# Performance work log

Measured on AMD Instinct MI355X. Metric: run time of the kernel, lower is better.

The kernel has to match this reference:

```python
import jax, jax.numpy as jnp
import numpy as np

N_CLASSES = 3  # hardcoded in the original module (labels == 0/1/2)
EPS = 1e-12    # F.normalize default eps


def setup_inputs() -> dict:
    key = jax.random.key(0)
    k1, k2, k3 = jax.random.split(key, 3)
    query = jax.random.normal(k1, (32768, 256), dtype=jnp.float32)
    memory = jax.random.normal(k2, (3, 512, 256), dtype=jnp.float32)
    labels = jax.random.randint(k3, (32768,), 0, 3, dtype=jnp.int64)
    return {"query": query, "labels": labels, "memory": memory}


def reference(query, labels, memory):
    C, n_cells, d = memory.shape  # (3, 512, 256)
    # ---- read: cross-attention over all C*n_cells memory slots ----
    mem_flat = memory.reshape(C * n_cells, d)
    scores = jax.nn.softmax(query @ mem_flat.T, axis=1)  # (N, C*n_cells)
    q_read = scores @ mem_flat                           # (N, d) == the per-row loop, batched

    # ---- update (training path): masked softmax over queries per class ----
    def upd(c):
        mask = labels == c                               # (N,)
        logits = query @ memory[c].T                     # (N, n_cells)
        logits = jnp.where(mask[:, None], logits, -jnp.inf)
        sq = jax.nn.softmax(logits, axis=0)              # softmax over (masked) queries
        delta = sq.T @ query                             # (n_cells, d); zero rows contribute 0
        new = memory[c] + delta
        norm = jnp.maximum(jnp.linalg.norm(new, axis=1, keepdims=True), EPS)
        return new / norm                                # F.normalize over dim=1

    new_mem = jnp.stack([upd(c) for c in range(C)])      # C is a small fixed constant (3)
    return q_read, jax.lax.stop_gradient(new_mem)        # original detaches updated memory
```

## Files before the change

### kernel.cpp

```cpp
#include <hip/hip_runtime.h>
#include <math.h>

#define NQ    32768
#define DDIM  256
#define NCLS  3
#define CELLS 512
#define STOT  1536
#define BK    32

typedef __attribute__((ext_vector_type(8)))  short bf16x8;
typedef __attribute__((ext_vector_type(16))) float f32x16;

#define ROWF(r) (((r) & 3) + 8 * ((r) >> 2) + 4 * lh)

#define PIPE_WAIT_BAR(N) asm volatile("s_waitcnt vmcnt(" #N ")\n\ts_barrier" ::: "memory")
#define PIPE_BAR()       asm volatile("s_barrier" ::: "memory")

__device__ __forceinline__ f32x16 mfma16(bf16x8 a, bf16x8 b, f32x16 c) {
    return __builtin_amdgcn_mfma_f32_32x32x16_bf16(a, b, c, 0, 0, 0);
}
__device__ __forceinline__ unsigned short f2bf(float f) {
    const unsigned u = __float_as_uint(f);
    return (unsigned short)((u + 0x7FFFu + ((u >> 16) & 1u)) >> 16);
}
__device__ __forceinline__ float bf2f(unsigned short b) {
    return __uint_as_float(((unsigned)b) << 16);
}
__device__ __forceinline__ float sum16(bf16x8 w0, bf16x8 w1) {
    float s = 0.f;
#pragma unroll
    for (int e = 0; e < 8; ++e)
        s += bf2f((unsigned short)w0[e]) + bf2f((unsigned short)w1[e]);
    return s;
}
__device__ __forceinline__ void gl16(const unsigned short* g, unsigned short* l) {
    __builtin_amdgcn_global_load_lds(
        (const __attribute__((address_space(1))) unsigned int*)g,
        (__attribute__((address_space(3))) unsigned int*)l, 16, 0, 0);
}

__global__ __launch_bounds__(256) void k_conv2(const float* __restrict__ Q,
        const float* __restrict__ M,
        unsigned short* __restrict__ Qhi, unsigned short* __restrict__ Qlo,
        unsigned short* __restrict__ QhiT, float* __restrict__ qn2,
        unsigned short* __restrict__ Mhi, unsigned short* __restrict__ Mlo,
        unsigned short* __restrict__ MhiT, float* __restrict__ mn2) {
    __shared__ unsigned short lh_s[64][65];
    const int bq = NQ / 64;
    const bool isQ = (int)blockIdx.x < bq;
    const float* src        = isQ ? Q    : M;
    unsigned short* hi      = isQ ? Qhi  : Mhi;
    unsigned short* lo      = isQ ? Qlo  : Mlo;
    unsigned short* hiT     = isQ ? QhiT : MhiT;
    float* sq               = isQ ? qn2  : mn2;
    const int R             = isQ ? NQ   : STOT;
    const int r0 = (isQ ? blockIdx.x : blockIdx.x - bq) * 64;
    const int k0 = blockIdx.y * 64, t = threadIdx.x;
#pragma unroll
    for (int it = 0; it < 4; ++it) {
        const int idx = t + 256 * it;
        const int rl = idx >> 4, kq = idx & 15;
        const float4 v = *(const float4*)(src + (size_t)(r0 + rl) * DDIM + k0 + kq * 4);
        const unsigned short h0 = f2bf(v.x), h1 = f2bf(v.y), h2 = f2bf(v.z), h3 = f2bf(v.w);
        const unsigned short l0 = f2bf(v.x - bf2f(h0)), l1 = f2bf(v.y - bf2f(h1));
        const unsigned short l2 = f2bf(v.z - bf2f(h2)), l3 = f2bf(v.w - bf2f(h3));
        ushort4 hv; hv.x = h0; hv.y = h1; hv.z = h2; hv.w = h3;
        ushort4 lv; lv.x = l0; lv.y = l1; lv.z = l2; lv.w = l3;
        *(ushort4*)(hi + (size_t)(r0 + rl) * DDIM + k0 + kq * 4) = hv;
        *(ushort4*)(lo + (size_t)(r0 + rl) * DDIM + k0 + kq * 4) = lv;
        lh_s[rl][kq * 4 + 0] = h0; lh_s[rl][kq * 4 + 1] = h1;
        lh_s[rl][kq * 4 + 2] = h2; lh_s[rl][kq * 4 + 3] = h3;
        float ssq = v.x * v.x + v.y * v.y + v.z * v.z + v.w * v.w;
        ssq += __shfl_xor(ssq, 1, 64);
        ssq += __shfl_xor(ssq, 2, 64);
        ssq += __shfl_xor(ssq, 4, 64);
        ssq += __shfl_xor(ssq, 8, 64);
        if (kq == 0) atomicAdd(&sq[r0 + rl], ssq);
    }
    __syncthreads();
#pragma unroll
    for (int it = 0; it < 16; ++it) {
        const int idx = t + 256 * it;
        const int kl = idx >> 6, rl = idx & 63;
        hiT[(size_t)(k0 + kl) * R + r0 + rl] = lh_s[rl][kl];
    }
}

__global__ __launch_bounds__(256) void k_pe(
        const unsigned short* __restrict__ Qhi, const unsigned short* __restrict__ Qlo,
        const unsigned short* __restrict__ Mhi, const unsigned short* __restrict__ Mlo,
        const int* __restrict__ labels, const float* __restrict__ qn2,
        const float* __restrict__ mn2,
        unsigned short* __restrict__ P, unsigned short* __restrict__ ET,
        float* __restrict__ rowsum, float* __restrict__ colsum,
        int ibase, int ch, int ipg) {
    __shared__ unsigned short sA[2][2][128][BK];
    __shared__ unsigned short sB[2][2][192][BK];
    typedef unsigned short trt[32][40];
    trt* trP = (trt*)&sA[0][0][0][0];
    trt* trE = trP + 4;

    const int t = threadIdx.x, lane = t & 63, wid = t >> 6;
    const int l31 = lane & 31, lh = lane >> 5;
    const int wi = wid >> 1, wj = wid & 1;
    int ib, jb;
    if (ipg > 0) {
        const int xcd = blockIdx.x & 7, s = blockIdx.x >> 3;
        jb = s & 7; ib = xcd * ipg + (s >> 3);
    } else { jb = blockIdx.x % 8; ib = blockIdx.x / 8; }
    const int iblk = ib * 128, jblk = jb * 192;
    const int iloc0 = iblk + wi * 64;
    const int j0    = jblk + wj * 96;

    const unsigned short* gA[2] = { Qhi + (size_t)(ibase + iblk) * DDIM,
                                    Qlo + (size_t)(ibase + iblk) * DDIM };
    const unsigned short* gB[2] = { Mhi + (size_t)jblk * DDIM,
                                    Mlo + (size_t)jblk * DDIM };
    auto STAGE = [&](int b, int k0) {
#pragma unroll
        for (int h = 0; h < 2; ++h) {
#pragma unroll
            for (int it = 0; it < 2; ++it) {
                const int c = wid * 128 + it * 64 + lane;
                const int r = c >> 2, o = ((c ^ (c >> 3)) & 3) * 8;
                gl16(gA[h] + (size_t)r * DDIM + k0 + o, &sA[b][h][0][0] + c * 8);
            }
#pragma unroll
            for (int it = 0; it < 3; ++it) {
                const int c = wid * 192 + it * 64 + lane;
                const int r = c >> 2, o = ((c ^ (c >> 3)) & 3) * 8;
                gl16(gB[h] + (size_t)r * DDIM + k0 + o, &sB[b][h][0][0] + c * 8);
            }
        }
    };

    f32x16 acc[2][3] = {};
    const int ra0 = wi * 64 + l31, ra1 = ra0 + 32;
    const int rb0 = wj * 96 + l31, rb1 = rb0 + 32, rb2 = rb0 + 64;
    const int swa = (ra0 >> 1) & 3;
    const int swb = (rb0 >> 1) & 3;
    auto COMPUTE = [&](int b) {
#pragma unroll
        for (int t16 = 0; t16 < 2; ++t16) {
            const int oc = t16 * 2 + lh;
            const int ka = (oc ^ swa) * 8, kb = (oc ^ swb) * 8;
            const bf16x8 a0h = *(const bf16x8*)&sA[b][0][ra0][ka];
            const bf16x8 a1h = *(const bf16x8*)&sA[b][0][ra1][ka];
            const bf16x8 a0l = *(const bf16x8*)&sA[b][1][ra0][ka];
            const bf16x8 a1l = *(const bf16x8*)&sA[b][1][ra1][ka];
            const bf16x8 b0h = *(const bf16x8*)&sB[b][0][rb0][kb];
            const bf16x8 b1h = *(const bf16x8*)&sB[b][0][rb1][kb];
            const bf16x8 b2h = *(const bf16x8*)&sB[b][0][rb2][kb];
            const bf16x8 b0l = *(const bf16x8*)&sB[b][1][rb0][kb];
            const bf16x8 b1l = *(const bf16x8*)&sB[b][1][rb1][kb];
            const bf16x8 b2l = *(const bf16x8*)&sB[b][1][rb2][kb];
            acc[0][0] = mfma16(a0h, b0h, acc[0][0]);
            acc[0][0] = mfma16(a0h, b0l, acc[0][0]);
            acc[0][0] = mfma16(a0l, b0h, acc[0][0]);
            acc[0][1] = mfma16(a0h, b1h, acc[0][1]);
            acc[0][1] = mfma16(a0h, b1l, acc[0][1]);
            acc[0][1] = mfma16(a0l, b1h, acc[0][1]);
            acc[0][2] = mfma16(a0h, b2h, acc[0][2]);
            acc[0][2] = mfma16(a0h, b2l, acc[0][2]);
            acc[0][2] = mfma16(a0l, b2h, acc[0][2]);
            acc[1][0] = mfma16(a1h, b0h, acc[1][0]);
            acc[1][0] = mfma16(a1h, b0l, acc[1][0]);
            acc[1][0] = mfma16(a1l, b0h, acc[1][0]);
            acc[1][1] = mfma16(a1h, b1h, acc[1][1]);
            acc[1][1] = mfma16(a1h, b1l, acc[1][1]);
            acc[1][1] = mfma16(a1l, b1h, acc[1][1]);
            acc[1][2] = mfma16(a1h, b2h, acc[1][2]);
            acc[1][2] = mfma16(a1h, b2l, acc[1][2]);
            acc[1][2] = mfma16(a1l, b2h, acc[1][2]);
        }
    };

    STAGE(0, 0);
    STAGE(1, BK);
    for (int s = 0; s < DDIM / BK - 1; ++s) {
        PIPE_WAIT_BAR(10);
        COMPUTE(s & 1);
        PIPE_BAR();
        if (s + 2 < DDIM / BK) STAGE(s & 1, (s + 2) * BK);
    }
    PIPE_WAIT_BAR(0);
    COMPUTE(1);
    __syncthreads();

    float em3[3];
#pragma unroll
    for (int tj = 0; tj < 3; ++tj)
        em3[tj] = __expf(96.0f - 6.0f * sqrtf(mn2[j0 + tj * 32 + l31]));

    float rsum[2] = {0.f, 0.f};
    float csum[3] = {0.f, 0.f, 0.f};
#pragma unroll
    for (int ti = 0; ti < 2; ++ti) {
        float qn[16], eq[16]; int lab[16];
        const int ig0 = ibase + iloc0 + ti * 32;
#pragma unroll
        for (int r = 0; r < 16; ++r) {
            const int ir = ig0 + ROWF(r);
            qn[r] = 6.0f * sqrtf(qn2[ir]);
            eq[r] = __expf(qn[r] - 96.0f);
            lab[r] = labels[ir];
        }
#pragma unroll
        for (int tj = 0; tj < 3; ++tj) {
            const int cblk = (j0 + tj * 32) >> 9;
            const float em = em3[tj];
#pragma unroll
            for (int r = 0; r < 16; r += 2) {
                const float p0 = __expf(acc[ti][tj][r] - qn[r]);
                const float p1 = __expf(acc[ti][tj][r + 1] - qn[r + 1]);
                trP[wid][ROWF(r)][l31]     = f2bf(p0);
                trP[wid][ROWF(r + 1)][l31] = f2bf(p1);
                const float e0 = (lab[r] == cblk)     ? p0 * eq[r] * em     : 0.0f;
                const float e1 = (lab[r + 1] == cblk) ? p1 * eq[r + 1] * em : 0.0f;
                const unsigned pk = (unsigned)f2bf(e0) | ((unsigned)f2bf(e1) << 16);
                *(unsigned*)&trE[wid][l31][ROWF(r)] = pk;
            }
            const int rr = lane >> 1, off = (lane & 1) * 16;
            {
                const unsigned short* lp = &trP[wid][rr][off];
                const bf16x8 w0 = *(const bf16x8*)(lp);
                const bf16x8 w1 = *(const bf16x8*)(lp + 8);
                unsigned short* prow = P + (size_t)(iloc0 + ti * 32 + rr) * STOT
                                         + j0 + tj * 32 + off;
                *(bf16x8*)(prow)     = w0;
                *(bf16x8*)(prow + 8) = w1;
                rsum[ti] += sum16(w0, w1);
            }
            {
                const unsigned short* lp = &trE[wid][rr][off];
                const bf16x8 w0 = *(const bf16x8*)(lp);
                const bf16x8 w1 = *(const bf16x8*)(lp + 8);
                unsigned short* erow = ET + (size_t)(j0 + tj * 32 + rr) * ch
                                          + iloc0 + ti * 32 + off;
                *(bf16x8*)(erow)     = w0;
                *(bf16x8*)(erow + 8) = w1;
                csum[tj] += sum16(w0, w1);
            }
        }
    }
    {
        const int rr = lane >> 1;
#pragma unroll
        for (int ti = 0; ti < 2; ++ti) {
            const float v = rsum[ti] + __shfl_xor(rsum[ti], 1, 64);
            if ((lane & 1) == 0)
                atomicAdd(&rowsum[ibase + iloc0 + ti * 32 + rr], v);
        }
#pragma unroll
        for (int tj = 0; tj < 3; ++tj) {
            const float v = csum[tj] + __shfl_xor(csum[tj], 1, 64);
            if ((lane & 1) == 0)
                atomicAdd(&colsum[j0 + tj * 32 + rr], v);
        }
    }
}

__global__ __launch_bounds__(256) void k_pv(const unsigned short* __restrict__ P,
        const unsigned short* __restrict__ MhiT, const float* __restrict__ rowsum,
        float* __restrict__ out, int ibase) {
    __shared__ unsigned short sP[2][128][64];
    __shared__ unsigned short sV[2][128][64];
    const int t = threadIdx.x, lane = t & 63, wid = t >> 6;
    const int l31 = lane & 31, lh = lane >> 5;
    const int wq = wid >> 1, wd = wid & 1;
    const int qblk = blockIdx.x * 128, dblk = blockIdx.y * 128;
    const unsigned short* gP = P + (size_t)qblk * STOT;
    const unsigned short* gV = MhiT + (size_t)dblk * STOT;

    auto STAGE = [&](int b, int k0) {
#pragma unroll
        for (int it = 0; it < 4; ++it) {
            const int c = wid * 256 + it * 64 + lane;
            const int r = c >> 3, o = ((c & 7) ^ (r & 7)) * 8;
            gl16(gP + (size_t)r * STOT + k0 + o, &sP[b][0][0] + c * 8);
            gl16(gV + (size_t)r * STOT + k0 + o, &sV[b][0][0] + c * 8);
        }
    };

    f32x16 acc[2][2] = {};
    const int rp0 = wq * 64 + l31, rp1 = rp0 + 32;
    const int rv0 = wd * 64 + l31, rv1 = rv0 + 32;
    auto COMPUTE = [&](int b) {
#pragma unroll
        for (int t16 = 0; t16 < 4; ++t16) {
            const int oc = t16 * 2 + lh;
            const bf16x8 a0 = *(const bf16x8*)&sP[b][rp0][(oc ^ (rp0 & 7)) * 8];
            const bf16x8 a1 = *(const bf16x8*)&sP[b][rp1][(oc ^ (rp1 & 7)) * 8];
            const bf16x8 b0 = *(const bf16x8*)&sV[b][rv0][(oc ^ (rv0 & 7)) * 8];
            const bf16x8 b1 = *(const bf16x8*)&sV[b][rv1][(oc ^ (rv1 & 7)) * 8];
            acc[0][0] = mfma16(a0, b0, acc[0][0]);
            acc[0][1] = mfma16(a0, b1, acc[0][1]);
            acc[1][0] = mfma16(a1, b0, acc[1][0]);
            acc[1][1] = mfma16(a1, b1, acc[1][1]);
        }
    };

    STAGE(0, 0);
    STAGE(1, 64);
    for (int s = 0; s < STOT / 64 - 1; ++s) {
        PIPE_WAIT_BAR(8);
        COMPUTE(s & 1);
        PIPE_BAR();
        if (s + 2 < STOT / 64) STAGE(s & 1, (s + 2) * 64);
    }
    PIPE_WAIT_BAR(0);
    COMPUTE(1);

    float riv[2][16];
#pragma unroll
    for (int tq = 0; tq < 2; ++tq)
#pragma unroll
        for (int r = 0; r < 16; ++r)
            riv[tq][r] = 1.f / rowsum[ibase + qblk + wq * 64 + tq * 32 + ROWF(r)];
#pragma unroll
    for (int tq = 0; tq < 2; ++tq) {
#pragma unroll
        for (int td = 0; td < 2; ++td) {
#pragma unroll
            for (int r = 0; r < 16; ++r) {
                const int ig = ibase + qblk + wq * 64 + tq * 32 + ROWF(r);
                const int od = dblk + wd * 64 + td * 32 + l31;
                out[(size_t)ig * DDIM + od] = acc[tq][td][r] * riv[tq][r];
            }
        }
    }
}

__global__ __launch_bounds__(256) void k_delta4(const unsigned short* __restrict__ ET,
        const unsigned short* __restrict__ QhiT,
        float* __restrict__ delta, int ibase, int ch, int ppx) {
    __shared__ unsigned short sE[2][128][64];
    __shared__ unsigned short sQ[2][128][64];
    const int t = threadIdx.x, lane = t & 63, wid = t >> 6;
    const int l31 = lane & 31, lh = lane >> 5;
    const int wj = wid >> 1, wd = wid & 1;
    int jb, db, kb;
    if (ppx > 0) {
        const int xcd = blockIdx.x & 7, s = blockIdx.x >> 3;
        jb = s % 12;
        const int pidx = xcd * ppx + s / 12;
        kb = pidx >> 1; db = pidx & 1;
    } else {
        jb = blockIdx.x % 12; db = (blockIdx.x / 12) & 1; kb = blockIdx.x / 24;
    }
    const int jblk = jb * 128, dblk = db * 128, i0 = kb * 1024;
    const int j0 = jblk + wj * 64, d0 = dblk + wd * 64;
    const unsigned short* gE = ET + (size_t)jblk * ch + i0;
    const unsigned short* gQ = QhiT + (size_t)dblk * NQ + ibase + i0;

    auto STAGE = [&](int b, int k0) {
#pragma unroll
        for (int it = 0; it < 4; ++it) {
            const int c = wid * 256 + it * 64 + lane;
            const int r = c >> 3, o = ((c & 7) ^ (r & 7)) * 8;
            gl16(gE + (size_t)r * ch + k0 + o, &sE[b][0][0] + c * 8);
            gl16(gQ + (size_t)r * NQ + k0 + o, &sQ[b][0][0] + c * 8);
        }
    };

    f32x16 acc[2][2] = {};
    const int re0 = wj * 64 + l31, re1 = re0 + 32;
    const int rq0 = wd * 64 + l31, rq1 = rq0 + 32;
    auto COMPUTE = [&](int b) {
#pragma unroll
        for (int t16 = 0; t16 < 4; ++t16) {
            const int oc = t16 * 2 + lh;
            const bf16x8 a0 = *(const bf16x8*)&sE[b][re0][(oc ^ (re0 & 7)) * 8];
            const bf16x8 a1 = *(const bf16x8*)&sE[b][re1][(oc ^ (re1 & 7)) * 8];
            const bf16x8 b0 = *(const bf16x8*)&sQ[b][rq0][(oc ^ (rq0 & 7)) * 8];
            const bf16x8 b1 = *(const bf16x8*)&sQ[b][rq1][(oc ^ (rq1 & 7)) * 8];
            acc[0][0] = mfma16(a0, b0, acc[0][0]);
            acc[0][1] = mfma16(a0, b1, acc[0][1]);
            acc[1][0] = mfma16(a1, b0, acc[1][0]);
            acc[1][1] = mfma16(a1, b1, acc[1][1]);
        }
    };

    STAGE(0, 0);
    STAGE(1, 64);
    for (int s = 0; s < 15; ++s) {
        PIPE_WAIT_BAR(8);
        COMPUTE(s & 1);
        PIPE_BAR();
        if (s + 2 < 16) STAGE(s & 1, (s + 2) * 64);
    }
    PIPE_WAIT_BAR(0);
    COMPUTE(1);

#pragma unroll
    for (int tj = 0; tj < 2; ++tj) {
#pragma unroll
        for (int td = 0; td < 2; ++td) {
#pragma unroll
            for (int r = 0; r < 16; ++r) {
                const int jr = j0 + tj * 32 + ROWF(r);
                atomicAdd(&delta[(size_t)jr * DDIM + d0 + td * 32 + l31], acc[tj][td][r]);
            }
        }
    }
}

__global__ void k_final(const float* __restrict__ M,
                        const float* __restrict__ delta,
                        const float* __restrict__ colsum,
                        float* __restrict__ out) {
    const int row  = blockIdx.x * 4 + (threadIdx.x >> 6);
    const int lane = threadIdx.x & 63;
    const float inv = 1.f / colsum[row];
    const float4 mv = *(const float4*)(M + (size_t)row * DDIM + lane * 4);
    const float4 dv = *(const float4*)(delta + (size_t)row * DDIM + lane * 4);
    float4 nv;
    nv.x = fmaf(dv.x, inv, mv.x);
    nv.y = fmaf(dv.y, inv, mv.y);
    nv.z = fmaf(dv.z, inv, mv.z);
    nv.w = fmaf(dv.w, inv, mv.w);
    float ss = nv.x * nv.x + nv.y * nv.y + nv.z * nv.z + nv.w * nv.w;
#pragma unroll
    for (int sh = 1; sh < 64; sh <<= 1) ss += __shfl_xor(ss, sh, 64);
    const float rn = 1.f / fmaxf(sqrtf(ss), 1e-12f);
    nv.x *= rn; nv.y *= rn; nv.z *= rn; nv.w *= rn;
    *(float4*)(out + (size_t)NQ * DDIM + (size_t)row * DDIM + lane * 4) = nv;
}

extern "C" void kernel_launch(void* const* d_in, const int* in_sizes, int n_in,
                              void* d_out, int out_size, void* d_ws, size_t ws_size,
                              hipStream_t stream) {
    const float* Q      = (const float*)d_in[0];
    const int*   labels = (const int*)d_in[1];
    const float* M      = (const float*)d_in[2];
    float* out = (float*)d_out;

    char* p = (char*)d_ws;
    float* colsum = (float*)p;          p += (size_t)STOT * 4;
    float* delta  = (float*)p;          p += (size_t)STOT * DDIM * 4;
    float* qn2    = (float*)p;          p += (size_t)NQ * 4;
    float* mn2    = (float*)p;          p += (size_t)STOT * 4;
    float* rowsum = (float*)p;          p += (size_t)NQ * 4;
    const size_t zero_bytes = (size_t)(p - (char*)d_ws);
    unsigned short* Qhi  = (unsigned short*)p; p += (size_t)NQ * DDIM * 2;
    unsigned short* Qlo  = (unsigned short*)p; p += (size_t)NQ * DDIM * 2;
    unsigned short* QhiT = (unsigned short*)p; p += (size_t)NQ * DDIM * 2;
    unsigned short* Mhi  = (unsigned short*)p; p += (size_t)STOT * DDIM * 2;
    unsigned short* Mlo  = (unsigned short*)p; p += (size_t)STOT * DDIM * 2;
    unsigned short* MhiT = (unsigned short*)p; p += (size_t)STOT * DDIM * 2;
    const size_t fixed_bytes = (size_t)(p - (char*)d_ws);

    int nch = 2;
    while (nch < 32 &&
           fixed_bytes + (size_t)(NQ / nch) * STOT * 2 * 2 > ws_size) nch <<= 1;
    const int ch = NQ / nch;
    unsigned short* Pbuf = (unsigned short*)p;
    unsigned short* ETb  = Pbuf + (size_t)ch * STOT;

    const int ipg    = ((ch / 128) % 8 == 0) ? (ch / 128) / 8 : 0;
    const int ksplit = ch / 1024;
    const int ppx    = ((2 * ksplit) % 8 == 0) ? (2 * ksplit) / 8 : 0;

    hipMemsetAsync(d_ws, 0, zero_bytes, stream);

    k_conv2<<<dim3(NQ / 64 + STOT / 64, 4), 256, 0, stream>>>(
        Q, M, Qhi, Qlo, QhiT, qn2, Mhi, Mlo, MhiT, mn2);

    for (int h = 0; h < nch; ++h) {
        const int ibase = h * ch;
        k_pe<<<8 * (ch / 128), 256, 0, stream>>>(Qhi, Qlo, Mhi, Mlo, labels,
                                                 qn2, mn2, Pbuf, ETb, rowsum, colsum,
                                                 ibase, ch, ipg);
        k_pv<<<dim3(ch / 128, 2), 256, 0, stream>>>(Pbuf, MhiT, rowsum, out, ibase);
        k_delta4<<<24 * ksplit, 256, 0, stream>>>(ETb, QhiT, delta, ibase, ch, ppx);
    }
    k_final<<<STOT / 4, 256, 0, stream>>>(M, delta, colsum, out);
}
```

Measured before the change: 266.4 us.

## Sort queries by label so delta GEMM skips zero-masked class blocks

Adds count and scatter kernels that build a label-sorted permutation of queries. Conversion gathers query rows in that order, and the PV output is scattered back through the index. The E matrix and the delta GEMM then touch only the contiguous K-range of each class's queries, which cuts that GEMM's work to about a third. It costs two extra small launches and atomics, an indirect output write, and a delta split that may be uneven across K.

```diff
diff --git a/kernel.cpp b/kernel.cpp
--- a/kernel.cpp
+++ b/kernel.cpp
@@ -39,8 +39,46 @@
         (__attribute__((address_space(3))) unsigned int*)l, 16, 0, 0);
 }
 
+__global__ __launch_bounds__(256) void k_count(const int* __restrict__ labels,
+        unsigned* __restrict__ cnt) {
+    const int i = blockIdx.x * 256 + threadIdx.x;
+    const int lane = threadIdx.x & 63;
+    const int c = labels[i];
+    const unsigned long long m0 = __ballot(c == 0), m1 = __ballot(c == 1);
+    if (lane == 0) {
+        const unsigned n0 = __popcll(m0), n1 = __popcll(m1);
+        atomicAdd(&cnt[0], n0);
+        atomicAdd(&cnt[1], n1);
+        atomicAdd(&cnt[2], 64u - n0 - n1);
+    }
+}
+
+__global__ __launch_bounds__(256) void k_scatter(const int* __restrict__ labels,
+        const unsigned* __restrict__ cnt, unsigned* __restrict__ wcnt,
+        int* __restrict__ idx) {
+    const int i = blockIdx.x * 256 + threadIdx.x;
+    const int lane = threadIdx.x & 63;
+    const int c = labels[i];
+    const unsigned long long m0 = __ballot(c == 0), m1 = __ballot(c == 1),
+                             m2 = __ballot(c == 2);
+    const unsigned long long mym = (c == 0) ? m0 : (c == 1) ? m1 : m2;
+    const unsigned long long ltm = ((unsigned long long)1 << lane) - 1;
+    const unsigned rank = __popcll(mym & ltm);
+    int b0 = 0, b1 = 0, b2 = 0;
+    if (lane == 0) {
+        b0 = (int)atomicAdd(&wcnt[0], __popcll(m0));
+        b1 = (int)atomicAdd(&wcnt[1], __popcll(m1));
+        b2 = (int)atomicAdd(&wcnt[2], __popcll(m2));
+    }
+    b0 = __shfl(b0, 0, 64); b1 = __shfl(b1, 0, 64); b2 = __shfl(b2, 0, 64);
+    const unsigned base = (c == 0) ? (unsigned)b0
+                        : (c == 1) ? cnt[0] + (unsigned)b1
+                                   : cnt[0] + cnt[1] + (unsigned)b2;
+    idx[base + rank] = i;
+}
+
 __global__ __launch_bounds__(256) void k_conv2(const float* __restrict__ Q,
-        const float* __restrict__ M,
+        const float* __restrict__ M, const int* __restrict__ idx,
         unsigned short* __restrict__ Qhi, unsigned short* __restrict__ Qlo,
         unsigned short* __restrict__ QhiT, float* __restrict__ qn2,
         unsigned short* __restrict__ Mhi, unsigned short* __restrict__ Mlo,
@@ -58,9 +96,10 @@
     const int k0 = blockIdx.y * 64, t = threadIdx.x;
 #pragma unroll
     for (int it = 0; it < 4; ++it) {
-        const int idx = t + 256 * it;
-        const int rl = idx >> 4, kq = idx & 15;
-        const float4 v = *(const float4*)(src + (size_t)(r0 + rl) * DDIM + k0 + kq * 4);
+        const int idxl = t + 256 * it;
+        const int rl = idxl >> 4, kq = idxl & 15;
+        const int orow = isQ ? idx[r0 + rl] : (r0 + rl);
+        const float4 v = *(const float4*)(src + (size_t)orow * DDIM + k0 + kq * 4);
         const unsigned short h0 = f2bf(v.x), h1 = f2bf(v.y), h2 = f2bf(v.z), h3 = f2bf(v.w);
         const unsigned short l0 = f2bf(v.x - bf2f(h0)), l1 = f2bf(v.y - bf2f(h1));
         const unsigned short l2 = f2bf(v.z - bf2f(h2)), l3 = f2bf(v.w - bf2f(h3));
@@ -80,8 +119,8 @@
     __syncthreads();
 #pragma unroll
     for (int it = 0; it < 16; ++it) {
-        const int idx = t + 256 * it;
-        const int kl = idx >> 6, rl = idx & 63;
+        const int idxl = t + 256 * it;
+        const int kl = idxl >> 6, rl = idxl & 63;
         hiT[(size_t)(k0 + kl) * R + r0 + rl] = lh_s[rl][kl];
     }
 }
@@ -89,7 +128,7 @@
 __global__ __launch_bounds__(256) void k_pe(
         const unsigned short* __restrict__ Qhi, const unsigned short* __restrict__ Qlo,
         const unsigned short* __restrict__ Mhi, const unsigned short* __restrict__ Mlo,
-        const int* __restrict__ labels, const float* __restrict__ qn2,
+        const unsigned* __restrict__ cnt, const float* __restrict__ qn2,
         const float* __restrict__ mn2,
         unsigned short* __restrict__ P, unsigned short* __restrict__ ET,
         float* __restrict__ rowsum, float* __restrict__ colsum,
@@ -187,6 +226,7 @@
     COMPUTE(1);
     __syncthreads();
 
+    const int sC1 = (int)cnt[0], sC2 = sC1 + (int)cnt[1];
     float em3[3];
 #pragma unroll
     for (int tj = 0; tj < 3; ++tj)
@@ -196,18 +236,23 @@
     float csum[3] = {0.f, 0.f, 0.f};
 #pragma unroll
     for (int ti = 0; ti < 2; ++ti) {
-        float qn[16], eq[16]; int lab[16];
+        float qn[16], eq[16];
         const int ig0 = ibase + iloc0 + ti * 32;
 #pragma unroll
         for (int r = 0; r < 16; ++r) {
             const int ir = ig0 + ROWF(r);
             qn[r] = 6.0f * sqrtf(qn2[ir]);
             eq[r] = __expf(qn[r] - 96.0f);
-            lab[r] = labels[ir];
         }
 #pragma unroll
         for (int tj = 0; tj < 3; ++tj) {
-            const int cblk = (j0 + tj * 32) >> 9;
+            const int c = (j0 + tj * 32) >> 9;
+            const int sc = (c == 0) ? 0 : (c == 1) ? sC1 : sC2;
+            const int ec = (c == 0) ? sC1 : (c == 1) ? sC2 : NQ;
+            const int lo = max(sc - ibase, 0), hi = min(ec - ibase, ch);
+            const int klo = lo & ~63, khi = (hi + 63) & ~63;
+            const int L0 = iloc0 + ti * 32;
+            const bool doE = (lo < hi) && (L0 < khi) && (L0 + 32 > klo);
             const float em = em3[tj];
 #pragma unroll
             for (int r = 0; r < 16; r += 2) {
@@ -215,10 +260,13 @@
                 const float p1 = __expf(acc[ti][tj][r + 1] - qn[r + 1]);
                 trP[wid][ROWF(r)][l31]     = f2bf(p0);
                 trP[wid][ROWF(r + 1)][l31] = f2bf(p1);
-                const float e0 = (lab[r] == cblk)     ? p0 * eq[r] * em     : 0.0f;
-                const float e1 = (lab[r + 1] == cblk) ? p1 * eq[r + 1] * em : 0.0f;
-                const unsigned pk = (unsigned)f2bf(e0) | ((unsigned)f2bf(e1) << 16);
-                *(unsigned*)&trE[wid][l31][ROWF(r)] = pk;
+                if (doE) {
+                    const int i0r = ig0 + ROWF(r), i1r = ig0 + ROWF(r + 1);
+                    const float e0 = (i0r >= sc && i0r < ec) ? p0 * eq[r] * em : 0.f;
+                    const float e1 = (i1r >= sc && i1r < ec) ? p1 * eq[r + 1] * em : 0.f;
+                    const unsigned pk = (unsigned)f2bf(e0) | ((unsigned)f2bf(e1) << 16);
+                    *(unsigned*)&trE[wid][l31][ROWF(r)] = pk;
+                }
             }
             const int rr = lane >> 1, off = (lane & 1) * 16;
             {
@@ -231,7 +279,7 @@
                 *(bf16x8*)(prow + 8) = w1;
                 rsum[ti] += sum16(w0, w1);
             }
-            {
+            if (doE) {
                 const unsigned short* lp = &trE[wid][rr][off];
                 const bf16x8 w0 = *(const bf16x8*)(lp);
                 const bf16x8 w1 = *(const bf16x8*)(lp + 8);
@@ -262,7 +310,7 @@
 
 __global__ __launch_bounds__(256) void k_pv(const unsigned short* __restrict__ P,
         const unsigned short* __restrict__ MhiT, const float* __restrict__ rowsum,
-        float* __restrict__ out, int ibase) {
+        const int* __restrict__ idx, float* __restrict__ out, int ibase) {
     __shared__ unsigned short sP[2][128][64];
     __shared__ unsigned short sV[2][128][64];
     const int t = threadIdx.x, lane = t & 63, wid = t >> 6;
@@ -323,17 +371,17 @@
         for (int td = 0; td < 2; ++td) {
 #pragma unroll
             for (int r = 0; r < 16; ++r) {
-                const int ig = ibase + qblk + wq * 64 + tq * 32 + ROWF(r);
+                const int sp = ibase + qblk + wq * 64 + tq * 32 + ROWF(r);
                 const int od = dblk + wd * 64 + td * 32 + l31;
-                out[(size_t)ig * DDIM + od] = acc[tq][td][r] * riv[tq][r];
+                out[(size_t)idx[sp] * DDIM + od] = acc[tq][td][r] * riv[tq][r];
             }
         }
     }
 }
 
 __global__ __launch_bounds__(256) void k_delta4(const unsigned short* __restrict__ ET,
-        const unsigned short* __restrict__ QhiT,
-        float* __restrict__ delta, int ibase, int ch, int ppx) {
+        const unsigned short* __restrict__ QhiT, const unsigned* __restrict__ cnt,
+        float* __restrict__ delta, int ibase, int ch, int ksplit, int ppx) {
     __shared__ unsigned short sE[2][128][64];
     __shared__ unsigned short sQ[2][128][64];
     const int t = threadIdx.x, lane = t & 63, wid = t >> 6;
@@ -348,18 +396,32 @@
     } else {
         jb = blockIdx.x % 12; db = (blockIdx.x / 12) & 1; kb = blockIdx.x / 24;
     }
-    const int jblk = jb * 128, dblk = db * 128, i0 = kb * 1024;
+    const int jblk = jb * 128, dblk = db * 128;
     const int j0 = jblk + wj * 64, d0 = dblk + wd * 64;
-    const unsigned short* gE = ET + (size_t)jblk * ch + i0;
-    const unsigned short* gQ = QhiT + (size_t)dblk * NQ + ibase + i0;
+
+    const int c = jblk >> 9;
+    const int sC1 = (int)cnt[0], sC2 = sC1 + (int)cnt[1];
+    const int sc = (c == 0) ? 0 : (c == 1) ? sC1 : sC2;
+    const int ec = (c == 0) ? sC1 : (c == 1) ? sC2 : NQ;
+    const int lo = max(sc - ibase, 0), hi = min(ec - ibase, ch);
+    if (lo >= hi) return;
+    const int klo = lo & ~63, khi = (hi + 63) & ~63;
+    const int itot = (khi - klo) >> 6;
+    const int per = (itot + ksplit - 1) / ksplit;
+    const int myn = min(per, itot - kb * per);
+    if (myn <= 0) return;
+    const int st = klo + kb * per * 64;
+
+    const unsigned short* gE = ET + (size_t)jblk * ch + st;
+    const unsigned short* gQ = QhiT + (size_t)dblk * NQ + ibase + st;
 
     auto STAGE = [&](int b, int k0) {
 #pragma unroll
         for (int it = 0; it < 4; ++it) {
-            const int c = wid * 256 + it * 64 + lane;
-            const int r = c >> 3, o = ((c & 7) ^ (r & 7)) * 8;
-            gl16(gE + (size_t)r * ch + k0 + o, &sE[b][0][0] + c * 8);
-            gl16(gQ + (size_t)r * NQ + k0 + o, &sQ[b][0][0] + c * 8);
+            const int cc = wid * 256 + it * 64 + lane;
+            const int r = cc >> 3, o = ((cc & 7) ^ (r & 7)) * 8;
+            gl16(gE + (size_t)r * ch + k0 + o, &sE[b][0][0] + cc * 8);
+            gl16(gQ + (size_t)r * NQ + k0 + o, &sQ[b][0][0] + cc * 8);
         }
     };
 
@@ -382,15 +444,15 @@
     };
 
     STAGE(0, 0);
-    STAGE(1, 64);
-    for (int s = 0; s < 15; ++s) {
+    if (myn > 1) STAGE(1, 64);
+    for (int s = 0; s < myn - 1; ++s) {
         PIPE_WAIT_BAR(8);
         COMPUTE(s & 1);
         PIPE_BAR();
-        if (s + 2 < 16) STAGE(s & 1, (s + 2) * 64);
+        if (s + 2 < myn) STAGE(s & 1, (s + 2) * 64);
     }
     PIPE_WAIT_BAR(0);
-    COMPUTE(1);
+    COMPUTE((myn - 1) & 1);
 
 #pragma unroll
     for (int tj = 0; tj < 2; ++tj) {
@@ -441,7 +503,10 @@
     float* qn2    = (float*)p;          p += (size_t)NQ * 4;
     float* mn2    = (float*)p;          p += (size_t)STOT * 4;
     float* rowsum = (float*)p;          p += (size_t)NQ * 4;
+    unsigned* cnt  = (unsigned*)p;      p += 4 * 4;
+    unsigned* wcnt = (unsigned*)p;      p += 4 * 4;
     const size_t zero_bytes = (size_t)(p - (char*)d_ws);
+    int* idx = (int*)p;                 p += (size_t)NQ * 4;
     unsigned short* Qhi  = (unsigned short*)p; p += (size_t)NQ * DDIM * 2;
     unsigned short* Qlo  = (unsigned short*)p; p += (size_t)NQ * DDIM * 2;
     unsigned short* QhiT = (unsigned short*)p; p += (size_t)NQ * DDIM * 2;
@@ -463,16 +528,19 @@
 
     hipMemsetAsync(d_ws, 0, zero_bytes, stream);
 
+    k_count<<<NQ / 256, 256, 0, stream>>>(labels, cnt);
+    k_scatter<<<NQ / 256, 256, 0, stream>>>(labels, cnt, wcnt, idx);
     k_conv2<<<dim3(NQ / 64 + STOT / 64, 4), 256, 0, stream>>>(
-        Q, M, Qhi, Qlo, QhiT, qn2, Mhi, Mlo, MhiT, mn2);
+        Q, M, idx, Qhi, Qlo, QhiT, qn2, Mhi, Mlo, MhiT, mn2);
 
     for (int h = 0; h < nch; ++h) {
         const int ibase = h * ch;
-        k_pe<<<8 * (ch / 128), 256, 0, stream>>>(Qhi, Qlo, Mhi, Mlo, labels,
+        k_pe<<<8 * (ch / 128), 256, 0, stream>>>(Qhi, Qlo, Mhi, Mlo, cnt,
                                                  qn2, mn2, Pbuf, ETb, rowsum, colsum,
                                                  ibase, ch, ipg);
-        k_pv<<<dim3(ch / 128, 2), 256, 0, stream>>>(Pbuf, MhiT, rowsum, out, ibase);
-        k_delta4<<<24 * ksplit, 256, 0, stream>>>(ETb, QhiT, delta, ibase, ch, ppx);
+        k_pv<<<dim3(ch / 128, 2), 256, 0, stream>>>(Pbuf, MhiT, rowsum, idx, out, ibase);
+        k_delta4<<<24 * ksplit, 256, 0, stream>>>(ETb, QhiT, cnt, delta,
+                                                  ibase, ch, ksplit, ppx);
     }
     k_final<<<STOT / 4, 256, 0, stream>>>(M, delta, colsum, out);
 }
```

Result: slower. 308.3 us (+15.7%).
